# Performance work log

Hardware: AMD Instinct MI355X
Metric: run time of the kernel (lower is better)

## Reference

```python
import jax, jax.numpy as jnp
import numpy as np

B, N, F = 32, 64, 128          # batch, num_nodes, n_in_node
K, H, M, NH = 4, 256, 256, 256 # edge_types, msg_hid, msg_out, n_hid
E = N * (N - 1)                # fully-connected directed edges = 4032


def setup_inputs() -> dict:
    key = jax.random.key(0)
    ks = jax.random.split(key, 12)
    inputs = jax.random.normal(ks[0], (B, N, F), dtype=jnp.float32)
    # soft edge-type assignment per edge (rows sum to 1, as in NRI)
    rel_type = jax.nn.softmax(jax.random.normal(ks[1], (B, E, K), dtype=jnp.float32), axis=-1)
    # one-hot receiver/sender matrices for all i != j pairs
    idx = np.array([(i, j) for i in range(N) for j in range(N) if i != j], dtype=np.int64)
    eye = np.eye(N, dtype=np.float32)
    rel_rec = jnp.asarray(eye[idx[:, 0]])   # [E, N]
    rel_send = jnp.asarray(eye[idx[:, 1]])  # [E, N]
    # per-edge-type message MLP weights (stacked over K): y = x @ W + b
    W1 = jax.random.normal(ks[2], (K, 2 * F, H), dtype=jnp.float32) / np.sqrt(2 * F)
    b1 = jnp.zeros((K, H), dtype=jnp.float32)
    W2 = jax.random.normal(ks[3], (K, H, M), dtype=jnp.float32) / np.sqrt(H)
    b2 = jnp.zeros((K, M), dtype=jnp.float32)
    # output MLP
    Wo1 = jax.random.normal(ks[4], (F + M, NH), dtype=jnp.float32) / np.sqrt(F + M)
    bo1 = jnp.zeros((NH,), dtype=jnp.float32)
    Wo2 = jax.random.normal(ks[5], (NH, NH), dtype=jnp.float32) / np.sqrt(NH)
    bo2 = jnp.zeros((NH,), dtype=jnp.float32)
    Wo3 = jax.random.normal(ks[6], (NH, F), dtype=jnp.float32) / np.sqrt(NH)
    bo3 = jnp.zeros((F,), dtype=jnp.float32)
    return {"inputs": inputs, "rel_type": rel_type, "rel_rec": rel_rec, "rel_send": rel_send,
            "W1": W1, "b1": b1, "W2": W2, "b2": b2,
            "Wo1": Wo1, "bo1": bo1, "Wo2": Wo2, "bo2": bo2, "Wo3": Wo3, "bo3": bo3}


def reference(inputs, rel_type, rel_rec, rel_send, W1, b1, W2, b2, Wo1, bo1, Wo2, bo2, Wo3, bo3):
    # gather node states to edges via one-hot matmul (as in the source)
    receivers = jnp.einsum('en,bnf->bef', rel_rec, inputs)   # [B,E,F]
    senders = jnp.einsum('en,bnf->bef', rel_send, inputs)    # [B,E,F]
    pre_msg = jnp.concatenate([receivers, senders], axis=-1)  # [B,E,2F]
    # per-edge-type 2-layer ReLU MLP, batched over the K edge types
    h = jax.nn.relu(jnp.einsum('bef,kfh->bkeh', pre_msg, W1) + b1[:, None, :])  # [B,K,E,H]
    msg = jax.nn.relu(jnp.einsum('bkeh,khm->bkem', h, W2) + b2[:, None, :])     # [B,K,E,M]
    # mask by soft edge type and accumulate over types (dropout p=0 -> identity)
    all_msgs = jnp.einsum('bkem,bek->bem', msg, rel_type)     # [B,E,M]
    # scatter-aggregate messages to receiver nodes via one-hot matmul
    agg_msgs = jnp.einsum('en,bem->bnm', rel_rec, all_msgs)   # [B,N,M]
    aug = jnp.concatenate([inputs, agg_msgs], axis=-1)        # [B,N,F+M]
    p = jax.nn.relu(aug @ Wo1 + bo1)
    p = jax.nn.relu(p @ Wo2 + bo2)
    p = p @ Wo3 + bo3
    return inputs + p
```

## Files before the change

kernel.cpp:

```cpp
#include <hip/hip_runtime.h>


#define B_ 32
#define N_ 64
#define F_ 128
#define K_ 4
#define E_ 4032

#define WS_W2T 0u
#define WS_R   524288u
#define WS_S   4718592u
#define WS_AGG 8912896u

typedef unsigned short u16;
typedef u16    u16x4  __attribute__((ext_vector_type(4)));
typedef u16    u16x8  __attribute__((ext_vector_type(8)));
typedef __bf16 bf16x8 __attribute__((ext_vector_type(8)));
typedef float  f32x4  __attribute__((ext_vector_type(4)));
typedef float  f32x16 __attribute__((ext_vector_type(16)));

__device__ __forceinline__ u16 f2bf(float f) {
    unsigned u; __builtin_memcpy(&u, &f, 4);
    return (u16)((u + 0x7FFFu + ((u >> 16) & 1u)) >> 16);
}
__device__ __forceinline__ float bf2f(u16 u) {
    unsigned v = ((unsigned)u) << 16;
    float f; __builtin_memcpy(&f, &v, 4); return f;
}

#define LBAR() do { \
    asm volatile("s_waitcnt lgkmcnt(0)" ::: "memory"); \
    __builtin_amdgcn_s_barrier(); \
    __builtin_amdgcn_sched_barrier(0); \
} while (0)

__global__ __launch_bounds__(256) void prep_rs_kernel(
    const float* __restrict__ W2, const float* __restrict__ x,
    const float* __restrict__ W1, const float* __restrict__ b1,
    u16* __restrict__ W2t, u16* __restrict__ R, u16* __restrict__ S)
{
    __shared__ u16 ldsA[64 * 136];
    __shared__ u16 ldsW[32 * 136];
    const int tid = threadIdx.x;

    if (blockIdx.x < 1024) {
        unsigned gid = blockIdx.x * 256u + tid;
        unsigned chunk = gid >> 13, r = gid & 8191u;
        unsigned g = r >> 11, n = (r >> 3) & 255u, e = r & 7u;
        unsigned k = chunk >> 3, kc = chunk & 7u, ks2 = g >> 1, lhh = g & 1u;
        unsigned kk = kc * 32u + ks2 * 16u + lhh * 8u + e;
        W2t[gid] = f2bf(W2[(k * 256u + kk) * 256u + n]);
        return;
    }

    const int lane = tid & 63, w = tid >> 6;
    const int quad = lane >> 4, mloc = lane & 15;
    const int bx = blockIdx.x - 1024;
    const int k = bx >> 6, half = (bx >> 5) & 1, b = bx & 31;

    for (int idx = tid; idx < 2048; idx += 256) {
        int row = idx >> 5, c4 = idx & 31;
        f32x4 v = *(const f32x4*)&x[(b * 64 + row) * 128 + c4 * 4];
        u16x4 o;
#pragma unroll
        for (int e = 0; e < 4; ++e) o[e] = f2bf(v[e]);
        *(u16x4*)&ldsA[row * 136 + c4 * 4] = o;
    }
    __syncthreads();

    bf16x8 aF[4];
#pragma unroll
    for (int ks = 0; ks < 4; ++ks)
        aF[ks] = *(const bf16x8*)&ldsA[(w * 16 + mloc) * 136 + quad * 8 + ks * 32];

    u16* dst = half ? S : R;
    for (int c = 0; c < 8; ++c) {
        __syncthreads();
        for (int idx = tid; idx < 4096; idx += 256) {
            int n = idx & 31, f = idx >> 5;
            ldsW[n * 136 + f] = f2bf(W1[(k * 256 + half * 128 + f) * 256 + c * 32 + n]);
        }
        __syncthreads();
#pragma unroll
        for (int nt = 0; nt < 2; ++nt) {
            f32x4 acc = (f32x4){0.f, 0.f, 0.f, 0.f};
            const int boff = (nt * 16 + mloc) * 136 + quad * 8;
#pragma unroll
            for (int ks = 0; ks < 4; ++ks)
                acc = __builtin_amdgcn_mfma_f32_16x16x32_bf16(
                    aF[ks], *(const bf16x8*)&ldsW[boff + ks * 32], acc, 0, 0, 0);
            const int n = c * 32 + nt * 16 + mloc;
            const float bias = half ? 0.f : b1[k * 256 + n];
#pragma unroll
            for (int r = 0; r < 4; ++r) {
                int row = w * 16 + quad * 4 + r;
                if (half) {
                    dst[((size_t)((k * 8 + c) * 2048 + b * 64 + row)) * 32 + nt * 16 + mloc]
                        = f2bf(acc[r] + bias);
                } else {
                    dst[((size_t)(k * 2048 + b * 64 + row)) * 256 + n] = f2bf(acc[r] + bias);
                }
            }
        }
    }
}

__global__ __launch_bounds__(256, 3) void edge11_kernel(
    const u16* __restrict__ R, const u16* __restrict__ S2,
    const float* __restrict__ rel, const u16* __restrict__ W2t,
    const float* __restrict__ b2, u16* __restrict__ aggb)
{
    __shared__ u16   Hs[32][64][8];
    __shared__ float Rf[4][256];
    __shared__ float rtS[4][64];

    const int tid  = threadIdx.x;
    const int lane = tid & 63;
    const int w    = tid >> 6;
    const int l31  = lane & 31;
    const int lh   = lane >> 5;
    const int bid  = ((blockIdx.x & 7) << 8) | (blockIdx.x >> 3);
    const int b    = bid >> 6;
    const int i    = bid & 63;

    {
        const int k = tid >> 6, j = tid & 63;
        float v = 0.f;
        if (j != i) v = rel[((size_t)(b * E_) + i * 63 + (j - (j > i))) * 4 + k];
        rtS[k][j] = v;
    }
    {
        const int k = tid >> 6, e4 = tid & 63;
        u16x4 t4 = *(const u16x4*)&R[((size_t)(k * 2048 + b * 64 + i)) * 256 + e4 * 4];
#pragma unroll
        for (int e = 0; e < 4; ++e) Rf[k][e4 * 4 + e] = bf2f(t4[e]);
    }
    __syncthreads();

    const u16* Wb = W2t + lh * 2048 + (w * 64 + l31) * 8;

    float amsg[2] = {0.f, 0.f};

    for (int kT = 0; kT < 4; ++kT) {
#pragma unroll
        for (int s = 0; s < 8; ++s) {
            u16x8 sv = *(const u16x8*)&S2[((size_t)((kT * 8 + s) * 2048 + b * 64 + lane)) * 32 + w * 8];
            const float* rp = &Rf[kT][s * 32 + w * 8];
            f32x4 r0 = *(const f32x4*)rp, r1 = *(const f32x4*)(rp + 4);
            bf16x8 o;
#pragma unroll
            for (int e = 0; e < 4; ++e) {
                o[e]     = (__bf16)fmaxf(r0[e] + bf2f(sv[e]),     0.f);
                o[4 + e] = (__bf16)fmaxf(r1[e] + bf2f(sv[4 + e]), 0.f);
            }
            *(bf16x8*)&Hs[s * 4 + w][lane][0] = o;
        }
        __syncthreads();

        f32x16 acc[2][2];
#pragma unroll
        for (int mt = 0; mt < 2; ++mt)
#pragma unroll
            for (int nt = 0; nt < 2; ++nt) acc[mt][nt] = (f32x16)(0.f);

#pragma unroll
        for (int kc = 0; kc < 8; ++kc) {
            const int it = kT * 8 + kc;
#pragma unroll
            for (int ks2 = 0; ks2 < 2; ++ks2) {
                const int g = kc * 4 + ks2 * 2 + lh;
                bf16x8 A0 = *(const bf16x8*)&Hs[g][l31][0];
                bf16x8 A1 = *(const bf16x8*)&Hs[g][32 + l31][0];
                const u16* wp = Wb + (size_t)it * 8192 + ks2 * 4096;
                bf16x8 B0 = *(const bf16x8*)(wp);
                bf16x8 B1 = *(const bf16x8*)(wp + 256);
                acc[0][0] = __builtin_amdgcn_mfma_f32_32x32x16_bf16(A0, B0, acc[0][0], 0, 0, 0);
                acc[0][1] = __builtin_amdgcn_mfma_f32_32x32x16_bf16(A0, B1, acc[0][1], 0, 0, 0);
                acc[1][0] = __builtin_amdgcn_mfma_f32_32x32x16_bf16(A1, B0, acc[1][0], 0, 0, 0);
                acc[1][1] = __builtin_amdgcn_mfma_f32_32x32x16_bf16(A1, B1, acc[1][1], 0, 0, 0);
            }
        }

#pragma unroll
        for (int nt = 0; nt < 2; ++nt) {
            const float bias = b2[kT * 256 + w * 64 + nt * 32 + l31];
#pragma unroll
            for (int mt = 0; mt < 2; ++mt) {
                float s = 0.f;
#pragma unroll
                for (int rq = 0; rq < 4; ++rq) {
                    f32x4 rt4 = *(const f32x4*)&rtS[kT][mt * 32 + rq * 8 + 4 * lh];
#pragma unroll
                    for (int e = 0; e < 4; ++e) {
                        float v = acc[mt][nt][rq * 4 + e] + bias;
                        v = v > 0.f ? v : 0.f;
                        s += rt4[e] * v;
                    }
                }
                amsg[nt] += s;
            }
        }
        __syncthreads();
    }

#pragma unroll
    for (int nt = 0; nt < 2; ++nt) {
        float s = amsg[nt] + __shfl_xor(amsg[nt], 32);
        if (lh == 0)
            aggb[(size_t)(b * 64 + i) * 256 + w * 64 + nt * 32 + l31] = f2bf(s);
    }
}

__global__ __launch_bounds__(256) void outmlp3_kernel(
    const float* __restrict__ x, const u16* __restrict__ aggb,
    const float* __restrict__ Wo1, const float* __restrict__ bo1,
    const float* __restrict__ Wo2, const float* __restrict__ bo2,
    const float* __restrict__ Wo3, const float* __restrict__ bo3,
    float* __restrict__ out)
{
    __shared__ u16 wch[4][256][8];
    __shared__ u16 p1S[32 * 264];
    __shared__ u16 p2S[32 * 264];
    const int tid = threadIdx.x, lane = tid & 63, w = tid >> 6;
    const int quad = lane >> 4, mloc = lane & 15;
    const int row0 = blockIdx.x * 32;

    {
        f32x4 acc[2][4];
#pragma unroll
        for (int mt = 0; mt < 2; ++mt)
#pragma unroll
            for (int nt = 0; nt < 4; ++nt) acc[mt][nt] = (f32x4){0.f, 0.f, 0.f, 0.f};
        float wr[32];
#pragma unroll
        for (int g = 0; g < 4; ++g)
#pragma unroll
            for (int e = 0; e < 8; ++e) wr[g * 8 + e] = Wo1[(g * 8 + e) * 256 + tid];
        for (int kk = 0; kk < 12; ++kk) {
            bf16x8 aF[2];
#pragma unroll
            for (int mt = 0; mt < 2; ++mt) {
                const int row = row0 + mt * 16 + mloc;
                if (kk < 4) {
                    u16x8 t;
#pragma unroll
                    for (int e = 0; e < 8; ++e) t[e] = f2bf(x[row * 128 + kk * 32 + quad * 8 + e]);
                    __builtin_memcpy(&aF[mt], &t, 16);
                } else {
                    aF[mt] = *(const bf16x8*)&aggb[(size_t)row * 256 + (kk - 4) * 32 + quad * 8];
                }
            }
#pragma unroll
            for (int g = 0; g < 4; ++g) {
                u16x8 o;
#pragma unroll
                for (int e = 0; e < 8; ++e) o[e] = f2bf(wr[g * 8 + e]);
                *(u16x8*)&wch[g][tid][0] = o;
            }
            if (kk + 1 < 12) {
#pragma unroll
                for (int g = 0; g < 4; ++g)
#pragma unroll
                    for (int e = 0; e < 8; ++e) wr[g * 8 + e] = Wo1[((kk + 1) * 32 + g * 8 + e) * 256 + tid];
            }
            LBAR();
#pragma unroll
            for (int nt = 0; nt < 4; ++nt) {
                bf16x8 bF = *(const bf16x8*)&wch[quad][w * 64 + nt * 16 + mloc][0];
#pragma unroll
                for (int mt = 0; mt < 2; ++mt)
                    acc[mt][nt] = __builtin_amdgcn_mfma_f32_16x16x32_bf16(aF[mt], bF, acc[mt][nt], 0, 0, 0);
            }
            LBAR();
        }
#pragma unroll
        for (int nt = 0; nt < 4; ++nt) {
            const int n = w * 64 + nt * 16 + mloc;
            const float bias = bo1[n];
#pragma unroll
            for (int mt = 0; mt < 2; ++mt)
#pragma unroll
                for (int r = 0; r < 4; ++r) {
                    float v = acc[mt][nt][r] + bias;
                    p1S[(mt * 16 + quad * 4 + r) * 264 + n] = f2bf(v > 0.f ? v : 0.f);
                }
        }
    }
    LBAR();
    {
        f32x4 acc[2][4];
#pragma unroll
        for (int mt = 0; mt < 2; ++mt)
#pragma unroll
            for (int nt = 0; nt < 4; ++nt) acc[mt][nt] = (f32x4){0.f, 0.f, 0.f, 0.f};
        float wr[32];
#pragma unroll
        for (int g = 0; g < 4; ++g)
#pragma unroll
            for (int e = 0; e < 8; ++e) wr[g * 8 + e] = Wo2[(g * 8 + e) * 256 + tid];
        for (int kk = 0; kk < 8; ++kk) {
            bf16x8 aF[2];
#pragma unroll
            for (int mt = 0; mt < 2; ++mt)
                aF[mt] = *(const bf16x8*)&p1S[(mt * 16 + mloc) * 264 + kk * 32 + quad * 8];
#pragma unroll
            for (int g = 0; g < 4; ++g) {
                u16x8 o;
#pragma unroll
                for (int e = 0; e < 8; ++e) o[e] = f2bf(wr[g * 8 + e]);
                *(u16x8*)&wch[g][tid][0] = o;
            }
            if (kk + 1 < 8) {
#pragma unroll
                for (int g = 0; g < 4; ++g)
#pragma unroll
                    for (int e = 0; e < 8; ++e) wr[g * 8 + e] = Wo2[((kk + 1) * 32 + g * 8 + e) * 256 + tid];
            }
            LBAR();
#pragma unroll
            for (int nt = 0; nt < 4; ++nt) {
                bf16x8 bF = *(const bf16x8*)&wch[quad][w * 64 + nt * 16 + mloc][0];
#pragma unroll
                for (int mt = 0; mt < 2; ++mt)
                    acc[mt][nt] = __builtin_amdgcn_mfma_f32_16x16x32_bf16(aF[mt], bF, acc[mt][nt], 0, 0, 0);
            }
            LBAR();
        }
#pragma unroll
        for (int nt = 0; nt < 4; ++nt) {
            const int n = w * 64 + nt * 16 + mloc;
            const float bias = bo2[n];
#pragma unroll
            for (int mt = 0; mt < 2; ++mt)
#pragma unroll
                for (int r = 0; r < 4; ++r) {
                    float v = acc[mt][nt][r] + bias;
                    p2S[(mt * 16 + quad * 4 + r) * 264 + n] = f2bf(v > 0.f ? v : 0.f);
                }
        }
    }
    LBAR();
    {
        f32x4 acc[2][2];
#pragma unroll
        for (int mt = 0; mt < 2; ++mt)
#pragma unroll
            for (int nt = 0; nt < 2; ++nt) acc[mt][nt] = (f32x4){0.f, 0.f, 0.f, 0.f};
        const int sn = tid & 127, sh = tid >> 7;
        float wr[16];
#pragma unroll
        for (int g2 = 0; g2 < 2; ++g2)
#pragma unroll
            for (int e = 0; e < 8; ++e) wr[g2 * 8 + e] = Wo3[((sh * 2 + g2) * 8 + e) * 128 + sn];
        for (int kk = 0; kk < 8; ++kk) {
            bf16x8 aF[2];
#pragma unroll
            for (int mt = 0; mt < 2; ++mt)
                aF[mt] = *(const bf16x8*)&p2S[(mt * 16 + mloc) * 264 + kk * 32 + quad * 8];
#pragma unroll
            for (int g2 = 0; g2 < 2; ++g2) {
                const int g = sh * 2 + g2;
                u16x8 o;
#pragma unroll
                for (int e = 0; e < 8; ++e) o[e] = f2bf(wr[g2 * 8 + e]);
                *(u16x8*)&wch[g][sn][0] = o;
            }
            if (kk + 1 < 8) {
#pragma unroll
                for (int g2 = 0; g2 < 2; ++g2)
#pragma unroll
                    for (int e = 0; e < 8; ++e)
                        wr[g2 * 8 + e] = Wo3[((kk + 1) * 32 + (sh * 2 + g2) * 8 + e) * 128 + sn];
            }
            LBAR();
#pragma unroll
            for (int nt = 0; nt < 2; ++nt) {
                bf16x8 bF = *(const bf16x8*)&wch[quad][w * 32 + nt * 16 + mloc][0];
#pragma unroll
                for (int mt = 0; mt < 2; ++mt)
                    acc[mt][nt] = __builtin_amdgcn_mfma_f32_16x16x32_bf16(aF[mt], bF, acc[mt][nt], 0, 0, 0);
            }
            LBAR();
        }
#pragma unroll
        for (int nt = 0; nt < 2; ++nt) {
            const int n = w * 32 + nt * 16 + mloc;
            const float bias = bo3[n];
#pragma unroll
            for (int mt = 0; mt < 2; ++mt)
#pragma unroll
                for (int r = 0; r < 4; ++r) {
                    const int grow = row0 + mt * 16 + quad * 4 + r;
                    out[grow * 128 + n] = x[grow * 128 + n] + acc[mt][nt][r] + bias;
                }
        }
    }
}

extern "C" void kernel_launch(void* const* d_in, const int* in_sizes, int n_in,
                              void* d_out, int out_size, void* d_ws, size_t ws_size,
                              hipStream_t stream) {
    const float* x   = (const float*)d_in[0];
    const float* rel = (const float*)d_in[1];
    const float* W1  = (const float*)d_in[4];
    const float* b1  = (const float*)d_in[5];
    const float* W2  = (const float*)d_in[6];
    const float* b2  = (const float*)d_in[7];
    const float* Wo1 = (const float*)d_in[8];
    const float* bo1 = (const float*)d_in[9];
    const float* Wo2 = (const float*)d_in[10];
    const float* bo2 = (const float*)d_in[11];
    const float* Wo3 = (const float*)d_in[12];
    const float* bo3 = (const float*)d_in[13];
    float* out = (float*)d_out;

    char* ws = (char*)d_ws;
    u16* W2t  = (u16*)(ws + WS_W2T);
    u16* R    = (u16*)(ws + WS_R);
    u16* S2   = (u16*)(ws + WS_S);
    u16* aggb = (u16*)(ws + WS_AGG);

    prep_rs_kernel<<<1280, 256, 0, stream>>>(W2, x, W1, b1, W2t, R, S2);
    edge11_kernel<<<2048, 256, 0, stream>>>(R, S2, rel, W2t, b2, aggb);
    outmlp3_kernel<<<64, 256, 0, stream>>>(x, aggb, Wo1, bo1, Wo2, bo2, Wo3, bo3, out);
}
```

Baseline: 207.1 us.

## Prefetch S2 and W2 tiles in registers; double warps in output MLP

```diff
diff --git a/kernel.cpp b/kernel.cpp
--- a/kernel.cpp
+++ b/kernel.cpp
@@ -105,7 +105,7 @@
     }
 }
 
-__global__ __launch_bounds__(256, 3) void edge11_kernel(
+__global__ __launch_bounds__(256, 3) void edge12_kernel(
     const u16* __restrict__ R, const u16* __restrict__ S2,
     const float* __restrict__ rel, const u16* __restrict__ W2t,
     const float* __restrict__ b2, u16* __restrict__ aggb)
@@ -135,6 +135,12 @@
 #pragma unroll
         for (int e = 0; e < 4; ++e) Rf[k][e4 * 4 + e] = bf2f(t4[e]);
     }
+
+    u16x8 sreg[8];
+#pragma unroll
+    for (int s = 0; s < 8; ++s)
+        sreg[s] = *(const u16x8*)&S2[((size_t)(s * 2048 + b * 64 + lane)) * 32 + w * 8];
+
     __syncthreads();
 
     const u16* Wb = W2t + lh * 2048 + (w * 64 + l31) * 8;
@@ -142,16 +148,22 @@
     float amsg[2] = {0.f, 0.f};
 
     for (int kT = 0; kT < 4; ++kT) {
+        bf16x8 Bb[2][2][2];
+#pragma unroll
+        for (int ks2 = 0; ks2 < 2; ++ks2) {
+            const u16* wp = Wb + (size_t)(kT * 8) * 8192 + ks2 * 4096;
+            Bb[0][ks2][0] = *(const bf16x8*)(wp);
+            Bb[0][ks2][1] = *(const bf16x8*)(wp + 256);
+        }
 #pragma unroll
         for (int s = 0; s < 8; ++s) {
-            u16x8 sv = *(const u16x8*)&S2[((size_t)((kT * 8 + s) * 2048 + b * 64 + lane)) * 32 + w * 8];
             const float* rp = &Rf[kT][s * 32 + w * 8];
             f32x4 r0 = *(const f32x4*)rp, r1 = *(const f32x4*)(rp + 4);
             bf16x8 o;
 #pragma unroll
             for (int e = 0; e < 4; ++e) {
-                o[e]     = (__bf16)fmaxf(r0[e] + bf2f(sv[e]),     0.f);
-                o[4 + e] = (__bf16)fmaxf(r1[e] + bf2f(sv[4 + e]), 0.f);
+                o[e]     = (__bf16)fmaxf(r0[e] + bf2f(sreg[s][e]),     0.f);
+                o[4 + e] = (__bf16)fmaxf(r1[e] + bf2f(sreg[s][4 + e]), 0.f);
             }
             *(bf16x8*)&Hs[s * 4 + w][lane][0] = o;
         }
@@ -165,19 +177,29 @@
 
 #pragma unroll
         for (int kc = 0; kc < 8; ++kc) {
-            const int it = kT * 8 + kc;
+            const int cur = kc & 1, nxt = cur ^ 1;
+            if (kc == 0 && kT < 3) {
+#pragma unroll
+                for (int s = 0; s < 8; ++s)
+                    sreg[s] = *(const u16x8*)&S2[((size_t)(((kT + 1) * 8 + s) * 2048 + b * 64 + lane)) * 32 + w * 8];
+            }
+            if (kc < 7) {
+#pragma unroll
+                for (int ks2 = 0; ks2 < 2; ++ks2) {
+                    const u16* wp = Wb + (size_t)(kT * 8 + kc + 1) * 8192 + ks2 * 4096;
+                    Bb[nxt][ks2][0] = *(const bf16x8*)(wp);
+                    Bb[nxt][ks2][1] = *(const bf16x8*)(wp + 256);
+                }
+            }
 #pragma unroll
             for (int ks2 = 0; ks2 < 2; ++ks2) {
                 const int g = kc * 4 + ks2 * 2 + lh;
                 bf16x8 A0 = *(const bf16x8*)&Hs[g][l31][0];
                 bf16x8 A1 = *(const bf16x8*)&Hs[g][32 + l31][0];
-                const u16* wp = Wb + (size_t)it * 8192 + ks2 * 4096;
-                bf16x8 B0 = *(const bf16x8*)(wp);
-                bf16x8 B1 = *(const bf16x8*)(wp + 256);
-                acc[0][0] = __builtin_amdgcn_mfma_f32_32x32x16_bf16(A0, B0, acc[0][0], 0, 0, 0);
-                acc[0][1] = __builtin_amdgcn_mfma_f32_32x32x16_bf16(A0, B1, acc[0][1], 0, 0, 0);
-                acc[1][0] = __builtin_amdgcn_mfma_f32_32x32x16_bf16(A1, B0, acc[1][0], 0, 0, 0);
-                acc[1][1] = __builtin_amdgcn_mfma_f32_32x32x16_bf16(A1, B1, acc[1][1], 0, 0, 0);
+                acc[0][0] = __builtin_amdgcn_mfma_f32_32x32x16_bf16(A0, Bb[cur][ks2][0], acc[0][0], 0, 0, 0);
+                acc[0][1] = __builtin_amdgcn_mfma_f32_32x32x16_bf16(A0, Bb[cur][ks2][1], acc[0][1], 0, 0, 0);
+                acc[1][0] = __builtin_amdgcn_mfma_f32_32x32x16_bf16(A1, Bb[cur][ks2][0], acc[1][0], 0, 0, 0);
+                acc[1][1] = __builtin_amdgcn_mfma_f32_32x32x16_bf16(A1, Bb[cur][ks2][1], acc[1][1], 0, 0, 0);
             }
         }
 
@@ -211,7 +233,7 @@
     }
 }
 
-__global__ __launch_bounds__(256) void outmlp3_kernel(
+__global__ __launch_bounds__(512) void outmlp4_kernel(
     const float* __restrict__ x, const u16* __restrict__ aggb,
     const float* __restrict__ Wo1, const float* __restrict__ bo1,
     const float* __restrict__ Wo2, const float* __restrict__ bo2,
@@ -221,178 +243,155 @@
     __shared__ u16 wch[4][256][8];
     __shared__ u16 p1S[32 * 264];
     __shared__ u16 p2S[32 * 264];
-    const int tid = threadIdx.x, lane = tid & 63, w = tid >> 6;
+    const int tid  = threadIdx.x, lane = tid & 63;
+    const int w8   = tid >> 6;
+    const int mh   = w8 >> 2;
+    const int w4   = w8 & 3;
     const int quad = lane >> 4, mloc = lane & 15;
     const int row0 = blockIdx.x * 32;
+    const int sg2  = (tid >> 8) * 2;
+    const int sn   = tid & 255;
 
     {
-        f32x4 acc[2][4];
-#pragma unroll
-        for (int mt = 0; mt < 2; ++mt)
-#pragma unroll
-            for (int nt = 0; nt < 4; ++nt) acc[mt][nt] = (f32x4){0.f, 0.f, 0.f, 0.f};
-        float wr[32];
-#pragma unroll
-        for (int g = 0; g < 4; ++g)
-#pragma unroll
-            for (int e = 0; e < 8; ++e) wr[g * 8 + e] = Wo1[(g * 8 + e) * 256 + tid];
+        f32x4 acc[4];
+#pragma unroll
+        for (int nt = 0; nt < 4; ++nt) acc[nt] = (f32x4){0.f, 0.f, 0.f, 0.f};
+        float wr[16];
+#pragma unroll
+        for (int g2 = 0; g2 < 2; ++g2)
+#pragma unroll
+            for (int e = 0; e < 8; ++e) wr[g2 * 8 + e] = Wo1[((sg2 + g2) * 8 + e) * 256 + sn];
         for (int kk = 0; kk < 12; ++kk) {
-            bf16x8 aF[2];
-#pragma unroll
-            for (int mt = 0; mt < 2; ++mt) {
-                const int row = row0 + mt * 16 + mloc;
+            bf16x8 aF;
+            {
+                const int row = row0 + mh * 16 + mloc;
                 if (kk < 4) {
                     u16x8 t;
 #pragma unroll
                     for (int e = 0; e < 8; ++e) t[e] = f2bf(x[row * 128 + kk * 32 + quad * 8 + e]);
-                    __builtin_memcpy(&aF[mt], &t, 16);
+                    __builtin_memcpy(&aF, &t, 16);
                 } else {
-                    aF[mt] = *(const bf16x8*)&aggb[(size_t)row * 256 + (kk - 4) * 32 + quad * 8];
+                    aF = *(const bf16x8*)&aggb[(size_t)row * 256 + (kk - 4) * 32 + quad * 8];
                 }
             }
 #pragma unroll
-            for (int g = 0; g < 4; ++g) {
+            for (int g2 = 0; g2 < 2; ++g2) {
                 u16x8 o;
 #pragma unroll
-                for (int e = 0; e < 8; ++e) o[e] = f2bf(wr[g * 8 + e]);
-                *(u16x8*)&wch[g][tid][0] = o;
+                for (int e = 0; e < 8; ++e) o[e] = f2bf(wr[g2 * 8 + e]);
+                *(u16x8*)&wch[sg2 + g2][sn][0] = o;
             }
             if (kk + 1 < 12) {
 #pragma unroll
-                for (int g = 0; g < 4; ++g)
-#pragma unroll
-                    for (int e = 0; e < 8; ++e) wr[g * 8 + e] = Wo1[((kk + 1) * 32 + g * 8 + e) * 256 + tid];
+                for (int g2 = 0; g2 < 2; ++g2)
+#pragma unroll
+                    for (int e = 0; e < 8; ++e)
+                        wr[g2 * 8 + e] = Wo1[((kk + 1) * 32 + (sg2 + g2) * 8 + e) * 256 + sn];
             }
             LBAR();
 #pragma unroll
             for (int nt = 0; nt < 4; ++nt) {
-                bf16x8 bF = *(const bf16x8*)&wch[quad][w * 64 + nt * 16 + mloc][0];
-#pragma unroll
-                for (int mt = 0; mt < 2; ++mt)
-                    acc[mt][nt] = __builtin_amdgcn_mfma_f32_16x16x32_bf16(aF[mt], bF, acc[mt][nt], 0, 0, 0);
+                bf16x8 bF = *(const bf16x8*)&wch[quad][w4 * 64 + nt * 16 + mloc][0];
+                acc[nt] = __builtin_amdgcn_mfma_f32_16x16x32_bf16(aF, bF, acc[nt], 0, 0, 0);
             }
             LBAR();
         }
 #pragma unroll
         for (int nt = 0; nt < 4; ++nt) {
-            const int n = w * 64 + nt * 16 + mloc;
+            const int n = w4 * 64 + nt * 16 + mloc;
             const float bias = bo1[n];
 #pragma unroll
-            for (int mt = 0; mt < 2; ++mt)
-#pragma unroll
-                for (int r = 0; r < 4; ++r) {
-                    float v = acc[mt][nt][r] + bias;
-                    p1S[(mt * 16 + quad * 4 + r) * 264 + n] = f2bf(v > 0.f ? v : 0.f);
-                }
+            for (int r = 0; r < 4; ++r) {
+                float v = acc[nt][r] + bias;
+                p1S[(mh * 16 + quad * 4 + r) * 264 + n] = f2bf(v > 0.f ? v : 0.f);
+            }
         }
     }
     LBAR();
     {
-        f32x4 acc[2][4];
-#pragma unroll
-        for (int mt = 0; mt < 2; ++mt)
-#pragma unroll
-            for (int nt = 0; nt < 4; ++nt) acc[mt][nt] = (f32x4){0.f, 0.f, 0.f, 0.f};
-        float wr[32];
-#pragma unroll
-        for (int g = 0; g < 4; ++g)
-#pragma unroll
-            for (int e = 0; e < 8; ++e) wr[g * 8 + e] = Wo2[(g * 8 + e) * 256 + tid];
+        f32x4 acc[4];
+#pragma unroll
+        for (int nt = 0; nt < 4; ++nt) acc[nt] = (f32x4){0.f, 0.f, 0.f, 0.f};
+        float wr[16];
+#pragma unroll
+        for (int g2 = 0; g2 < 2; ++g2)
+#pragma unroll
+            for (int e = 0; e < 8; ++e) wr[g2 * 8 + e] = Wo2[((sg2 + g2) * 8 + e) * 256 + sn];
         for (int kk = 0; kk < 8; ++kk) {
-            bf16x8 aF[2];
-#pragma unroll
-            for (int mt = 0; mt < 2; ++mt)
-                aF[mt] = *(const bf16x8*)&p1S[(mt * 16 + mloc) * 264 + kk * 32 + quad * 8];
-#pragma unroll
-            for (int g = 0; g < 4; ++g) {
+            bf16x8 aF = *(const bf16x8*)&p1S[(mh * 16 + mloc) * 264 + kk * 32 + quad * 8];
+#pragma unroll
+            for (int g2 = 0; g2 < 2; ++g2) {
                 u16x8 o;
 #pragma unroll
-                for (int e = 0; e < 8; ++e) o[e] = f2bf(wr[g * 8 + e]);
-                *(u16x8*)&wch[g][tid][0] = o;
+                for (int e = 0; e < 8; ++e) o[e] = f2bf(wr[g2 * 8 + e]);
+                *(u16x8*)&wch[sg2 + g2][sn][0] = o;
             }
             if (kk + 1 < 8) {
 #pragma unroll
-                for (int g = 0; g < 4; ++g)
-#pragma unroll
-                    for (int e = 0; e < 8; ++e) wr[g * 8 + e] = Wo2[((kk + 1) * 32 + g * 8 + e) * 256 + tid];
+                for (int g2 = 0; g2 < 2; ++g2)
+#pragma unroll
+                    for (int e = 0; e < 8; ++e)
+                        wr[g2 * 8 + e] = Wo2[((kk + 1) * 32 + (sg2 + g2) * 8 + e) * 256 + sn];
             }
             LBAR();
 #pragma unroll
             for (int nt = 0; nt < 4; ++nt) {
-                bf16x8 bF = *(const bf16x8*)&wch[quad][w * 64 + nt * 16 + mloc][0];
-#pragma unroll
-                for (int mt = 0; mt < 2; ++mt)
-                    acc[mt][nt] = __builtin_amdgcn_mfma_f32_16x16x32_bf16(aF[mt], bF, acc[mt][nt], 0, 0, 0);
+                bf16x8 bF = *(const bf16x8*)&wch[quad][w4 * 64 + nt * 16 + mloc][0];
+                acc[nt] = __builtin_amdgcn_mfma_f32_16x16x32_bf16(aF, bF, acc[nt], 0, 0, 0);
             }
             LBAR();
         }
 #pragma unroll
         for (int nt = 0; nt < 4; ++nt) {
-            const int n = w * 64 + nt * 16 + mloc;
+            const int n = w4 * 64 + nt * 16 + mloc;
             const float bias = bo2[n];
 #pragma unroll
-            for (int mt = 0; mt < 2; ++mt)
-#pragma unroll
-                for (int r = 0; r < 4; ++r) {
-                    float v = acc[mt][nt][r] + bias;
-                    p2S[(mt * 16 + quad * 4 + r) * 264 + n] = f2bf(v > 0.f ? v : 0.f);
-                }
+            for (int r = 0; r < 4; ++r) {
+                float v = acc[nt][r] + bias;
+                p2S[(mh * 16 + quad * 4 + r) * 264 + n] = f2bf(v > 0.f ? v : 0.f);
+            }
         }
     }
     LBAR();
     {
-        f32x4 acc[2][2];
-#pragma unroll
-        for (int mt = 0; mt < 2; ++mt)
-#pragma unroll
-            for (int nt = 0; nt < 2; ++nt) acc[mt][nt] = (f32x4){0.f, 0.f, 0.f, 0.f};
-        const int sn = tid & 127, sh = tid >> 7;
-        float wr[16];
-#pragma unroll
-        for (int g2 = 0; g2 < 2; ++g2)
-#pragma unroll
-            for (int e = 0; e < 8; ++e) wr[g2 * 8 + e] = Wo3[((sh * 2 + g2) * 8 + e) * 128 + sn];
+        f32x4 acc[2];
+#pragma unroll
+        for (int nt = 0; nt < 2; ++nt) acc[nt] = (f32x4){0.f, 0.f, 0.f, 0.f};
+        const int sg3 = tid >> 7;
+        const int sn3 = tid & 127;
+        float wr[8];
+#pragma unroll
+        for (int e = 0; e < 8; ++e) wr[e] = Wo3[(sg3 * 8 + e) * 128 + sn3];
         for (int kk = 0; kk < 8; ++kk) {
-            bf16x8 aF[2];
-#pragma unroll
-            for (int mt = 0; mt < 2; ++mt)
-                aF[mt] = *(const bf16x8*)&p2S[(mt * 16 + mloc) * 264 + kk * 32 + quad * 8];
-#pragma unroll
-            for (int g2 = 0; g2 < 2; ++g2) {
-                const int g = sh * 2 + g2;
+            bf16x8 aF = *(const bf16x8*)&p2S[(mh * 16 + mloc) * 264 + kk * 32 + quad * 8];
+            {
                 u16x8 o;
 #pragma unroll
-                for (int e = 0; e < 8; ++e) o[e] = f2bf(wr[g2 * 8 + e]);
-                *(u16x8*)&wch[g][sn][0] = o;
+                for (int e = 0; e < 8; ++e) o[e] = f2bf(wr[e]);
+                *(u16x8*)&wch[sg3][sn3][0] = o;
             }
             if (kk + 1 < 8) {
 #pragma unroll
-                for (int g2 = 0; g2 < 2; ++g2)
-#pragma unroll
-                    for (int e = 0; e < 8; ++e)
-                        wr[g2 * 8 + e] = Wo3[((kk + 1) * 32 + (sh * 2 + g2) * 8 + e) * 128 + sn];
+                for (int e = 0; e < 8; ++e)
+                    wr[e] = Wo3[((kk + 1) * 32 + sg3 * 8 + e) * 128 + sn3];
             }
             LBAR();
 #pragma unroll
             for (int nt = 0; nt < 2; ++nt) {
-                bf16x8 bF = *(const bf16x8*)&wch[quad][w * 32 + nt * 16 + mloc][0];
-#pragma unroll
-                for (int mt = 0; mt < 2; ++mt)
-                    acc[mt][nt] = __builtin_amdgcn_mfma_f32_16x16x32_bf16(aF[mt], bF, acc[mt][nt], 0, 0, 0);
+                bf16x8 bF = *(const bf16x8*)&wch[quad][w4 * 32 + nt * 16 + mloc][0];
+                acc[nt] = __builtin_amdgcn_mfma_f32_16x16x32_bf16(aF, bF, acc[nt], 0, 0, 0);
             }
             LBAR();
         }
 #pragma unroll
         for (int nt = 0; nt < 2; ++nt) {
-            const int n = w * 32 + nt * 16 + mloc;
+            const int n = w4 * 32 + nt * 16 + mloc;
             const float bias = bo3[n];
 #pragma unroll
-            for (int mt = 0; mt < 2; ++mt)
-#pragma unroll
-                for (int r = 0; r < 4; ++r) {
-                    const int grow = row0 + mt * 16 + quad * 4 + r;
-                    out[grow * 128 + n] = x[grow * 128 + n] + acc[mt][nt][r] + bias;
-                }
+            for (int r = 0; r < 4; ++r) {
+                const int grow = row0 + mh * 16 + quad * 4 + r;
+                out[grow * 128 + n] = x[grow * 128 + n] + acc[nt][r] + bias;
+            }
         }
     }
 }
@@ -421,6 +420,6 @@
     u16* aggb = (u16*)(ws + WS_AGG);
 
     prep_rs_kernel<<<1280, 256, 0, stream>>>(W2, x, W1, b1, W2t, R, S2);
-    edge11_kernel<<<2048, 256, 0, stream>>>(R, S2, rel, W2t, b2, aggb);
-    outmlp3_kernel<<<64, 256, 0, stream>>>(x, aggb, Wo1, bo1, Wo2, bo2, Wo3, bo3, out);
-}
+    edge12_kernel<<<2048, 256, 0, stream>>>(R, S2, rel, W2t, b2, aggb);
+    outmlp4_kernel<<<64, 512, 0, stream>>>(x, aggb, Wo1, bo1, Wo2, bo2, Wo3, bo3, out);
+}
```

New measurement: 196.1 us. -5.3%, faster.
